# Kernel tuning notes

Hardware: AMD Instinct MI355X
Metric: run time of the kernel (lower is better)

The kernel has to match this reference:

```python
import jax, jax.numpy as jnp
import numpy as np

B, S, H, FD, FL = 2, 2048, 1024, 3072, 3072
MAX_SPAN = 30
LAM = 0.4
MAX_K = int(S * LAM)  # static upper bound on top-k spans (819)
NEG = -10000.0
LN_EPS = 1e-5


def _mlp(x, W, b, g, be):
    # FullyConnectedLayer: Linear -> GELU(erf) -> LayerNorm (dropout = eval identity)
    h = jax.nn.gelu(x @ W + b, approximate=False)
    mu = jnp.mean(h, axis=-1, keepdims=True)
    var = jnp.var(h, axis=-1, keepdims=True)
    return (h - mu) / jnp.sqrt(var + LN_EPS) * g + be


def _mask_tensor(t, m):
    # s2e mask_tensor: additive -1e4 on masked entries, then clamp
    return jnp.clip(t + (1.0 - m) * NEG, NEG, -NEG)


def setup_inputs() -> dict:
    key = jax.random.key(0)
    ks = iter(jax.random.split(key, 32))
    w = lambda shape: jax.random.normal(next(ks), shape, jnp.float32) * 0.02
    inp = {
        "input_emb": jax.random.normal(next(ks), (B, S, H), jnp.float32),
        "input_masks": jnp.ones((B, S), jnp.int32),
    }
    for p, F in [("sm", FD), ("em", FD), ("sc", FL), ("ec", FL)]:
        inp[p + "_W"] = w((H, F))
        inp[p + "_b"] = jnp.zeros((F,), jnp.float32)
        inp[p + "_g"] = jnp.ones((F,), jnp.float32)
        inp[p + "_be"] = jnp.zeros((F,), jnp.float32)
    inp["cls_s_W"] = w((FD,)); inp["cls_s_b"] = jnp.zeros((), jnp.float32)
    inp["cls_e_W"] = w((FD,)); inp["cls_e_b"] = jnp.zeros((), jnp.float32)
    inp["s2e_W"] = w((FD, FD)); inp["s2e_b"] = jnp.zeros((FD,), jnp.float32)
    for p in ["a_ss", "a_ee", "a_se", "a_es"]:
        inp[p + "_W"] = w((FL, FL))
        inp[p + "_b"] = jnp.zeros((FL,), jnp.float32)
    return inp


def reference(input_emb, input_masks,
              sm_W, sm_b, sm_g, sm_be, em_W, em_b, em_g, em_be,
              sc_W, sc_b, sc_g, sc_be, ec_W, ec_b, ec_g, ec_be,
              cls_s_W, cls_s_b, cls_e_W, cls_e_b, s2e_W, s2e_b,
              a_ss_W, a_ss_b, a_ee_W, a_ee_b, a_se_W, a_se_b, a_es_W, a_es_b):
    # start/end representations
    sm = _mlp(input_emb, sm_W, sm_b, sm_g, sm_be)  # [B,S,FD]
    em = _mlp(input_emb, em_W, em_b, em_g, em_be)  # [B,S,FD]
    sc = _mlp(input_emb, sc_W, sc_b, sc_g, sc_be)  # [B,S,FL]
    ec = _mlp(input_emb, ec_W, ec_b, ec_g, ec_be)  # [B,S,FL]

    # mention scores: joint bilinear + broadcast start/end unary scores
    s_sc = sm @ cls_s_W + cls_s_b  # [B,S]
    e_sc = em @ cls_e_W + cls_e_b  # [B,S]
    joint = jnp.einsum('bsd,btd->bst', sm @ s2e_W + s2e_b, em)  # [B,S,S]
    mention = joint + s_sc[:, :, None] + e_sc[:, None, :]

    # triu(0) & tril(max_span_len-1) band mask
    ii = jnp.arange(S)
    d = ii[None, :] - ii[:, None]  # end - start
    band = ((d >= 0) & (d < MAX_SPAN)).astype(mention.dtype)
    mention = _mask_tensor(mention, band[None])

    # top-k over flattened S*S scores, per-example k via span_mask
    k = (input_masks.sum(-1).astype(jnp.float32) * LAM).astype(jnp.int32)  # [B]
    flat = mention.reshape(B, -1)
    _, top_idx = jax.lax.top_k(flat, MAX_K)  # [B,MAX_K]
    span_mask = (jnp.arange(MAX_K)[None, :] < k[:, None]).astype(jnp.int32)
    idx = top_idx * span_mask + (1 - span_mask) * (S * S - 1)
    sidx = jnp.sort(idx, axis=-1)
    starts = sidx // S  # [B,MAX_K]
    ends = sidx % S
    tms = jnp.take_along_axis(flat, sidx, axis=-1)  # [B,MAX_K]
    pair = tms[:, :, None] + tms[:, None, :]  # [B,MAX_K,MAX_K]

    # gather coref reps at top-k span boundaries
    tks = jnp.take_along_axis(sc, starts[:, :, None], axis=1)  # [B,MAX_K,FL]
    tke = jnp.take_along_axis(ec, ends[:, :, None], axis=1)    # [B,MAX_K,FL]

    coref = (jnp.einsum('bkd,bjd->bkj', tks @ a_ss_W + a_ss_b, tks)
             + jnp.einsum('bkd,bjd->bkj', tke @ a_ee_W + a_ee_b, tke)
             + jnp.einsum('bkd,bjd->bkj', tks @ a_se_W + a_se_b, tke)
             + jnp.einsum('bkd,bjd->bkj', tke @ a_es_W + a_es_b, tks))

    final = pair + coref
    amask = jnp.tril(jnp.ones((MAX_K, MAX_K), final.dtype), -1)[None]
    amask = amask * span_mask[:, :, None].astype(final.dtype)
    final = _mask_tensor(final, amask)
    final = jnp.concatenate([final, jnp.zeros((B, MAX_K, 1), final.dtype)], axis=-1)
    return final
```

## Files before the change

### kernel.cpp

```cpp
#include <hip/hip_runtime.h>
#include <hip/hip_bf16.h>
#include <math.h>

#define S_LEN 2048
#define BATCH 2
#define HDIM 1024
#define FDIM 3072
#define MAXK 819
#define MAXSPAN 30
#define NEGV -10000.0f

typedef __attribute__((ext_vector_type(8))) short short8;
typedef __attribute__((ext_vector_type(4))) float f32x4;
typedef __hip_bfloat16 hb;

__device__ __forceinline__ float gelu_f(float x) {
  return 0.5f * x * (1.0f + erff(x * 0.70710678118654752440f));
}

__device__ __forceinline__ unsigned short bf_bits(float x) {
  hb b = __float2bfloat16(x);
  return *reinterpret_cast<unsigned short*>(&b);
}
__device__ __forceinline__ float bf_back(unsigned short u) {
  hb b = *reinterpret_cast<hb*>(&u);
  return __bfloat162float(b);
}

__device__ __forceinline__ void gload16(const void* g, void* l) {
  __builtin_amdgcn_global_load_lds(
      (const __attribute__((address_space(1))) void*)g,
      (__attribute__((address_space(3))) void*)l, 16, 0, 0);
}

__global__ __launch_bounds__(256) void gemm_fast1(
    const hb* __restrict__ A, const hb* __restrict__ B,
    const float* __restrict__ bias, const float* __restrict__ bias2,
    void* __restrict__ Cv,
    int M, int N, int K, int lda, int ldb, int ldc,
    long long sA, long long sB, long long sC,
    int act, int out_mode, int kspl)
{
  const int zb = blockIdx.z / kspl, zk = blockIdx.z - zb * kspl;
  A += (long long)zb * sA + (long long)zk * K;
  B += (long long)zb * sB + (long long)zk * K;
  const long long cbase = (long long)blockIdx.z * sC;
  const float* bp = (bias2 && zb) ? bias2 : bias;
  const int bm = blockIdx.y * 128, bn = blockIdx.x * 128;
  const int tid = threadIdx.x;
  const int lane = tid & 63;
  const int wv = tid >> 6, wr = wv >> 1, wc = wv & 1;
  const int lrow = lane & 15, lk = lane >> 4;
  __shared__ __align__(16) hb As[128 * 128];
  __shared__ __align__(16) hb Bs[128 * 128];

  const int srow = tid >> 4;
  const int sc8 = tid & 15;
  const int sslot = (sc8 - srow) & 15;

  f32x4 acc[4][4];
#pragma unroll
  for (int mi = 0; mi < 4; ++mi)
#pragma unroll
    for (int ni = 0; ni < 4; ++ni) acc[mi][ni] = (f32x4){0.f, 0.f, 0.f, 0.f};

  long long aoff[8], boff[8];
#pragma unroll
  for (int it = 0; it < 8; ++it) {
    int gm = bm + srow + it * 16; if (gm > M - 1) gm = M - 1;
    int gn = bn + srow + it * 16; if (gn > N - 1) gn = N - 1;
    aoff[it] = (long long)gm * lda + sslot * 8;
    boff[it] = (long long)gn * ldb + sslot * 8;
  }

  for (int k0 = 0; k0 < K; k0 += 128) {
#pragma unroll
    for (int it = 0; it < 8; ++it)
      gload16(A + aoff[it] + k0, &As[(tid + it * 256) * 8]);
#pragma unroll
    for (int it = 0; it < 8; ++it)
      gload16(B + boff[it] + k0, &Bs[(tid + it * 256) * 8]);
    __syncthreads();
#pragma unroll
    for (int ks = 0; ks < 4; ++ks) {
      const int sa = ((ks * 4 + lk + lrow) & 15) * 8;
      short8 a[4], b[4];
#pragma unroll
      for (int mi = 0; mi < 4; ++mi)
        a[mi] = *(const short8*)&As[(wr * 64 + mi * 16 + lrow) * 128 + sa];
#pragma unroll
      for (int ni = 0; ni < 4; ++ni)
        b[ni] = *(const short8*)&Bs[(wc * 64 + ni * 16 + lrow) * 128 + sa];
#pragma unroll
      for (int mi = 0; mi < 4; ++mi)
#pragma unroll
        for (int ni = 0; ni < 4; ++ni)
          acc[mi][ni] = __builtin_amdgcn_mfma_f32_16x16x32_bf16(
              a[mi], b[ni], acc[mi][ni], 0, 0, 0);
    }
    __syncthreads();
  }

  float* Cf = (float*)Cv;
  hb* Cb = (hb*)Cv;
#pragma unroll
  for (int mi = 0; mi < 4; ++mi) {
#pragma unroll
    for (int ni = 0; ni < 4; ++ni) {
#pragma unroll
      for (int q = 0; q < 4; ++q) {
        int gm = bm + wr * 64 + mi * 16 + lk * 4 + q;
        int gn = bn + wc * 64 + ni * 16 + lrow;
        if (gm < M && gn < N) {
          float v = acc[mi][ni][q];
          if (bp)   v += bp[gn];
          if (act)  v = gelu_f(v);
          long long off = cbase + (long long)gm * ldc + gn;
          if (out_mode == 1) Cb[off] = __float2bfloat16(v);
          else               Cf[off] = v;
        }
      }
    }
  }
}

__global__ __launch_bounds__(256) void gemm_fast3(
    const hb* __restrict__ Ah, const hb* __restrict__ Al,
    const hb* __restrict__ Bh, const hb* __restrict__ Bl,
    const float* __restrict__ bias, void* __restrict__ Cv, void* __restrict__ Cv2,
    int M, int N, int K, int lda, int ldb, int ldc, int act, int out_mode)
{
  const int bm = blockIdx.y * 128, bn = blockIdx.x * 128;
  const int tid = threadIdx.x;
  const int lane = tid & 63;
  const int wv = tid >> 6, wr = wv >> 1, wc = wv & 1;
  const int lrow = lane & 15, lk = lane >> 4;
  __shared__ __align__(16) hb AsH[128 * 64];
  __shared__ __align__(16) hb AsL[128 * 64];
  __shared__ __align__(16) hb BsH[128 * 64];
  __shared__ __align__(16) hb BsL[128 * 64];

  const int srow = tid >> 3;
  const int sc8 = tid & 7;
  const int sslot = (sc8 - srow) & 7;

  f32x4 acc[4][4];
#pragma unroll
  for (int mi = 0; mi < 4; ++mi)
#pragma unroll
    for (int ni = 0; ni < 4; ++ni) acc[mi][ni] = (f32x4){0.f, 0.f, 0.f, 0.f};

  long long aoff[4], boff[4];
#pragma unroll
  for (int it = 0; it < 4; ++it) {
    int gm = bm + srow + it * 32; if (gm > M - 1) gm = M - 1;
    int gn = bn + srow + it * 32; if (gn > N - 1) gn = N - 1;
    aoff[it] = (long long)gm * lda + sslot * 8;
    boff[it] = (long long)gn * ldb + sslot * 8;
  }

  for (int k0 = 0; k0 < K; k0 += 64) {
#pragma unroll
    for (int it = 0; it < 4; ++it) {
      gload16(Ah + aoff[it] + k0, &AsH[(tid + it * 256) * 8]);
      gload16(Al + aoff[it] + k0, &AsL[(tid + it * 256) * 8]);
      gload16(Bh + boff[it] + k0, &BsH[(tid + it * 256) * 8]);
      gload16(Bl + boff[it] + k0, &BsL[(tid + it * 256) * 8]);
    }
    __syncthreads();
#pragma unroll
    for (int ks = 0; ks < 2; ++ks) {
      const int sa = ((ks * 4 + lk + lrow) & 7) * 8;
      short8 aH[4], aL[4], bH[4], bL[4];
#pragma unroll
      for (int mi = 0; mi < 4; ++mi) {
        int r = (wr * 64 + mi * 16 + lrow) * 64 + sa;
        aH[mi] = *(const short8*)&AsH[r];
        aL[mi] = *(const short8*)&AsL[r];
      }
#pragma unroll
      for (int ni = 0; ni < 4; ++ni) {
        int r = (wc * 64 + ni * 16 + lrow) * 64 + sa;
        bH[ni] = *(const short8*)&BsH[r];
        bL[ni] = *(const short8*)&BsL[r];
      }
#pragma unroll
      for (int mi = 0; mi < 4; ++mi)
#pragma unroll
        for (int ni = 0; ni < 4; ++ni) {
          acc[mi][ni] = __builtin_amdgcn_mfma_f32_16x16x32_bf16(
              aH[mi], bH[ni], acc[mi][ni], 0, 0, 0);
          acc[mi][ni] = __builtin_amdgcn_mfma_f32_16x16x32_bf16(
              aL[mi], bH[ni], acc[mi][ni], 0, 0, 0);
          acc[mi][ni] = __builtin_amdgcn_mfma_f32_16x16x32_bf16(
              aH[mi], bL[ni], acc[mi][ni], 0, 0, 0);
        }
    }
    __syncthreads();
  }

  float* Cf = (float*)Cv;
  hb* Cb = (hb*)Cv;
  hb* Cb2 = (hb*)Cv2;
#pragma unroll
  for (int mi = 0; mi < 4; ++mi) {
#pragma unroll
    for (int ni = 0; ni < 4; ++ni) {
#pragma unroll
      for (int q = 0; q < 4; ++q) {
        int gm = bm + wr * 64 + mi * 16 + lk * 4 + q;
        int gn = bn + wc * 64 + ni * 16 + lrow;
        if (gm < M && gn < N) {
          float v = acc[mi][ni][q];
          if (bias) v += bias[gn];
          if (act)  v = gelu_f(v);
          long long off = (long long)gm * ldc + gn;
          if (out_mode == 2) {
            unsigned short h = bf_bits(v);
            unsigned short l = bf_bits(v - bf_back(h));
            Cb[off] = *reinterpret_cast<hb*>(&h);
            Cb2[off] = *reinterpret_cast<hb*>(&l);
          } else {
            Cf[off] = v;
          }
        }
      }
    }
  }
}

__global__ __launch_bounds__(256) void bandmm(
    const hb* __restrict__ Phi, const hb* __restrict__ Plo,
    const hb* __restrict__ Ehi, const hb* __restrict__ Elo,
    float* __restrict__ partial)
{
  const int s0 = blockIdx.x * 64;
  const int kq = blockIdx.y;
  const int b = blockIdx.z;
  const int tid = threadIdx.x;
  const int lane = tid & 63;
  const int wv = tid >> 6, wr = wv >> 1, wc = wv & 1;
  const int lrow = lane & 15, lk = lane >> 4;
  __shared__ __align__(16) hb As[64 * 64];
  __shared__ __align__(16) hb Bs[96 * 64];

  f32x4 acc[2][3];
#pragma unroll
  for (int mi = 0; mi < 2; ++mi)
#pragma unroll
    for (int ni = 0; ni < 3; ++ni) acc[mi][ni] = (f32x4){0.f, 0.f, 0.f, 0.f};

  const long long Pbase = (long long)(b * S_LEN) * FDIM;
  long long aoff[2], boff[3];
#pragma unroll
  for (int it = 0; it < 2; ++it) {
    int row = (tid + it * 256) >> 3;
    aoff[it] = Pbase + (long long)(s0 + row) * FDIM + (tid & 7) * 8;
  }
#pragma unroll
  for (int it = 0; it < 3; ++it) {
    int row = (tid + it * 256) >> 3;
    int t = s0 + row; if (t > S_LEN - 1) t = S_LEN - 1;
    boff[it] = Pbase + (long long)t * FDIM + (tid & 7) * 8;
  }

  const int kbeg = kq * (FDIM / 4), kend = kbeg + FDIM / 4;
  for (int t3 = 0; t3 < 3; ++t3) {
    const hb* Ap = (t3 == 1) ? Plo : Phi;
    const hb* Bp = (t3 == 2) ? Elo : Ehi;
    for (int k0 = kbeg; k0 < kend; k0 += 64) {
#pragma unroll
      for (int it = 0; it < 2; ++it)
        gload16(Ap + aoff[it] + k0, &As[(tid + it * 256) * 8]);
#pragma unroll
      for (int it = 0; it < 3; ++it)
        gload16(Bp + boff[it] + k0, &Bs[(tid + it * 256) * 8]);
      __syncthreads();
#pragma unroll
      for (int ks = 0; ks < 2; ++ks) {
        short8 a[2], bb[3];
#pragma unroll
        for (int mi = 0; mi < 2; ++mi)
          a[mi] = *(const short8*)&As[(wr * 32 + mi * 16 + lrow) * 64 + ks * 32 + lk * 8];
#pragma unroll
        for (int ni = 0; ni < 3; ++ni)
          bb[ni] = *(const short8*)&Bs[(wc * 48 + ni * 16 + lrow) * 64 + ks * 32 + lk * 8];
#pragma unroll
        for (int mi = 0; mi < 2; ++mi)
#pragma unroll
          for (int ni = 0; ni < 3; ++ni)
            acc[mi][ni] = __builtin_amdgcn_mfma_f32_16x16x32_bf16(
                a[mi], bb[ni], acc[mi][ni], 0, 0, 0);
      }
      __syncthreads();
    }
  }

#pragma unroll
  for (int mi = 0; mi < 2; ++mi) {
#pragma unroll
    for (int ni = 0; ni < 3; ++ni) {
#pragma unroll
      for (int q = 0; q < 4; ++q) {
        int i = wr * 32 + mi * 16 + lk * 4 + q;
        int n = wc * 48 + ni * 16 + lrow;
        int d = n - i;
        if (d >= 0 && d < 32) {
          long long off = (((long long)(kq * 2 + b)) * S_LEN + (s0 + i)) * 32 + d;
          partial[off] = acc[mi][ni][q];
        }
      }
    }
  }
}

__global__ __launch_bounds__(256) void band_reduce(
    const float* __restrict__ partial, const float* __restrict__ ssc,
    const float* __restrict__ esc, float* __restrict__ band)
{
  int idx = blockIdx.x * 256 + threadIdx.x;
  if (idx >= BATCH * S_LEN * 32) return;
  int d = idx & 31;
  int s = (idx >> 5) & (S_LEN - 1);
  int b = idx >> 16;
  int t = s + d;
  float v;
  if (d < MAXSPAN && t < S_LEN) {
    float sum = 0.f;
#pragma unroll
    for (int kq = 0; kq < 4; ++kq)
      sum += partial[(((long long)(kq * 2 + b)) * S_LEN + s) * 32 + d];
    sum += ssc[b * S_LEN + s] + esc[b * S_LEN + t];
    v = fminf(fmaxf(sum, NEGV), -NEGV);
  } else {
    v = -3.0e38f;
  }
  band[idx] = v;
}

__global__ __launch_bounds__(256) void prep_split(
    const float* __restrict__ emb, hb* __restrict__ hi, hb* __restrict__ lo,
    long long n4, int nb_split,
    const float* __restrict__ W, hb* __restrict__ WhiT, hb* __restrict__ WloT,
    int K, int N)
{
  if ((int)blockIdx.x < nb_split) {
    long long i = (long long)blockIdx.x * 256 + threadIdx.x;
    if (i >= n4) return;
    float4 v = ((const float4*)emb)[i];
    unsigned short h[4], l[4];
    float vv[4] = {v.x, v.y, v.z, v.w};
#pragma unroll
    for (int j = 0; j < 4; ++j) {
      h[j] = bf_bits(vv[j]);
      l[j] = bf_bits(vv[j] - bf_back(h[j]));
    }
    ((uint2*)hi)[i] = *(uint2*)h;
    ((uint2*)lo)[i] = *(uint2*)l;
    return;
  }
  __shared__ float t[32][33];
  int idx = blockIdx.x - nb_split;
  int xb = idx % (N / 32), yb = idx / (N / 32);
  int k0 = yb * 32, n0 = xb * 32;
  int tx = threadIdx.x & 31, ty = threadIdx.x >> 5;
#pragma unroll
  for (int r = 0; r < 4; ++r)
    t[ty + r * 8][tx] = W[(long long)(k0 + ty + r * 8) * N + (n0 + tx)];
  __syncthreads();
#pragma unroll
  for (int r = 0; r < 4; ++r) {
    int n = n0 + ty + r * 8;
    float v = t[tx][ty + r * 8];
    unsigned short h = bf_bits(v);
    unsigned short l = bf_bits(v - bf_back(h));
    WhiT[(long long)n * K + k0 + tx] = *reinterpret_cast<hb*>(&h);
    WloT[(long long)n * K + k0 + tx] = *reinterpret_cast<hb*>(&l);
  }
}

__global__ __launch_bounds__(256) void splitT_mat(
    const float* __restrict__ src, hb* __restrict__ hiT, hb* __restrict__ loT,
    int K, int N)
{
  __shared__ float t[32][33];
  int k0 = blockIdx.y * 32, n0 = blockIdx.x * 32;
  int tx = threadIdx.x & 31, ty = threadIdx.x >> 5;
#pragma unroll
  for (int r = 0; r < 4; ++r)
    t[ty + r * 8][tx] = src[(long long)(k0 + ty + r * 8) * N + (n0 + tx)];
  __syncthreads();
#pragma unroll
  for (int r = 0; r < 4; ++r) {
    int n = n0 + ty + r * 8;
    float v = t[tx][ty + r * 8];
    unsigned short h = bf_bits(v);
    unsigned short l = bf_bits(v - bf_back(h));
    hiT[(long long)n * K + k0 + tx] = *reinterpret_cast<hb*>(&h);
    loT[(long long)n * K + k0 + tx] = *reinterpret_cast<hb*>(&l);
  }
}

__global__ __launch_bounds__(256) void ln_split_dot(
    const float* __restrict__ src, hb* __restrict__ hi, hb* __restrict__ lo,
    const float* __restrict__ g, const float* __restrict__ be,
    const float* __restrict__ w, const float* __restrict__ wb,
    float* __restrict__ dot_out)
{
  __shared__ float row[FDIM];
  __shared__ double scr[4];
  __shared__ double sh_mu, sh_rstd;
  const long long r = blockIdx.x;
  const float* p = src + r * FDIM;
  const int tid = threadIdx.x;

  double s = 0.0;
#pragma unroll
  for (int pp = 0; pp < 3; ++pp) {
    int c4 = pp * 256 + tid;
    float4 v = *(const float4*)(p + c4 * 4);
    *(float4*)&row[c4 * 4] = v;
    s += (double)v.x + (double)v.y + (double)v.z + (double)v.w;
  }
#pragma unroll
  for (int off = 32; off; off >>= 1) s += __shfl_down(s, off, 64);
  if ((tid & 63) == 0) scr[tid >> 6] = s;
  __syncthreads();
  if (tid == 0) sh_mu = (scr[0] + scr[1] + scr[2] + scr[3]) / FDIM;
  __syncthreads();
  double mu = sh_mu;
  double vs = 0.0;
#pragma unroll
  for (int pp = 0; pp < 12; ++pp) {
    double d = (double)row[pp * 256 + tid] - mu;
    vs += d * d;
  }
#pragma unroll
  for (int off = 32; off; off >>= 1) vs += __shfl_down(vs, off, 64);
  __syncthreads();
  if ((tid & 63) == 0) scr[tid >> 6] = vs;
  __syncthreads();
  if (tid == 0)
    sh_rstd = 1.0 / sqrt((scr[0] + scr[1] + scr[2] + scr[3]) / FDIM + 1e-5);
  __syncthreads();
  double rstd = sh_rstd;

  double dot = 0.0;
#pragma unroll
  for (int pp = 0; pp < 3; ++pp) {
    int c4 = pp * 256 + tid;
    float4 gv = *(const float4*)(g + c4 * 4);
    float4 bv = *(const float4*)(be + c4 * 4);
    float4 wv = *(const float4*)(w + c4 * 4);
    float xv[4];
    *(float4*)xv = *(const float4*)&row[c4 * 4];
    unsigned short hh[4], ll[4];
    float gg[4] = {gv.x, gv.y, gv.z, gv.w};
    float bb[4] = {bv.x, bv.y, bv.z, bv.w};
    float ww[4] = {wv.x, wv.y, wv.z, wv.w};
#pragma unroll
    for (int j = 0; j < 4; ++j) {
      float val = (float)(((double)xv[j] - mu) * rstd * (double)gg[j] + (double)bb[j]);
      dot += (double)val * (double)ww[j];
      hh[j] = bf_bits(val);
      ll[j] = bf_bits(val - bf_back(hh[j]));
    }
    *(uint2*)(hi + r * FDIM + c4 * 4) = *(uint2*)hh;
    *(uint2*)(lo + r * FDIM + c4 * 4) = *(uint2*)ll;
  }
#pragma unroll
  for (int off = 32; off; off >>= 1) dot += __shfl_down(dot, off, 64);
  __syncthreads();
  if ((tid & 63) == 0) scr[tid >> 6] = dot;
  __syncthreads();
  if (tid == 0)
    dot_out[r] = (float)(scr[0] + scr[1] + scr[2] + scr[3] + (double)wb[0]);
}

__global__ __launch_bounds__(256) void ln_rows_bf2(
    const float* __restrict__ src0, const float* __restrict__ src1,
    hb* __restrict__ dst0, hb* __restrict__ dst1,
    const float* __restrict__ g0, const float* __restrict__ g1,
    const float* __restrict__ be0, const float* __restrict__ be1,
    int n, long long lds_, long long ldd)
{
  const int sel = blockIdx.y;
  long long r = blockIdx.x;
  const float* p = (sel ? src1 : src0) + r * lds_;
  hb* d = (sel ? dst1 : dst0) + r * ldd;
  const float* g = sel ? g1 : g0;
  const float* be = sel ? be1 : be0;
  __shared__ double scratch[4];
  __shared__ double sh_mu, sh_rstd;
  double s = 0.0;
  for (int c = threadIdx.x; c < n; c += 256) s += (double)p[c];
#pragma unroll
  for (int off = 32; off; off >>= 1) s += __shfl_down(s, off, 64);
  if ((threadIdx.x & 63) == 0) scratch[threadIdx.x >> 6] = s;
  __syncthreads();
  if (threadIdx.x == 0) sh_mu = (scratch[0] + scratch[1] + scratch[2] + scratch[3]) / n;
  __syncthreads();
  double mu = sh_mu;
  double vs = 0.0;
  for (int c = threadIdx.x; c < n; c += 256) { double dd = (double)p[c] - mu; vs += dd * dd; }
#pragma unroll
  for (int off = 32; off; off >>= 1) vs += __shfl_down(vs, off, 64);
  __syncthreads();
  if ((threadIdx.x & 63) == 0) scratch[threadIdx.x >> 6] = vs;
  __syncthreads();
  if (threadIdx.x == 0)
    sh_rstd = 1.0 / sqrt((scratch[0] + scratch[1] + scratch[2] + scratch[3]) / n + 1e-5);
  __syncthreads();
  double rstd = sh_rstd;
  for (int c = threadIdx.x; c < n; c += 256)
    d[c] = __float2bfloat16(
        (float)(((double)p[c] - mu) * rstd * (double)g[c] + (double)be[c]));
}

__device__ __forceinline__ unsigned f2k(float f) {
  unsigned u = __float_as_uint(f);
  return (u & 0x80000000u) ? ~u : (u | 0x80000000u);
}

__device__ void bitonic1024(int* a) {
  const int tid = threadIdx.x;
  for (int sz = 2; sz <= 1024; sz <<= 1) {
    for (int st = sz >> 1; st > 0; st >>= 1) {
      __syncthreads();
      int j = tid ^ st;
      if (j > tid) {
        int x = a[tid], y = a[j];
        bool asc = (tid & sz) == 0;
        if ((x > y) == asc) { a[tid] = y; a[j] = x; }
      }
    }
  }
  __syncthreads();
}

__global__ __launch_bounds__(1024) void select_sort(
    const float* __restrict__ band, const int* __restrict__ masks,
    int* __restrict__ sidx, int* __restrict__ starts, int* __restrict__ ends,
    float* __restrict__ tms, int* __restrict__ kvals)
{
  const int b = blockIdx.x;
  const int tid = threadIdx.x;
  __shared__ int hist[256];
  __shared__ int sel[1024];
  __shared__ int eq[1024];
  __shared__ int sred[16];
  __shared__ int cvar[4];
  __shared__ int cnt_gt, cnt_eq;

  int msum = 0;
  for (int i = tid; i < S_LEN; i += 1024) msum += masks[b * S_LEN + i];
#pragma unroll
  for (int off = 32; off; off >>= 1) msum += __shfl_down(msum, off, 64);
  if ((tid & 63) == 0) sred[tid >> 6] = msum;
  __syncthreads();
  if (tid == 0) {
    int t = 0;
    for (int w = 0; w < 16; ++w) t += sred[w];
    cvar[2] = t;
  }
  __syncthreads();
  int kv = (int)((float)cvar[2] * 0.4f);
  if (kv > MAXK) kv = MAXK;
  if (kv < 0) kv = 0;

  const float* bb = band + (long long)b * (S_LEN * 32);
  const float4* b4 = (const float4*)bb;
  const int N4 = S_LEN * 8;
  unsigned prefix = 0u;
  int remaining = kv;

  if (kv > 0) {
    for (int byte = 3; byte >= 0; --byte) {
      if (tid < 256) hist[tid] = 0;
      __syncthreads();
      for (int i = tid; i < N4; i += 1024) {
        float4 v = b4[i];
        float vv[4] = {v.x, v.y, v.z, v.w};
#pragma unroll
        for (int j = 0; j < 4; ++j) {
          unsigned key = f2k(vv[j]);
          bool match = (byte == 3) ||
              ((key >> ((byte + 1) * 8)) == (prefix >> ((byte + 1) * 8)));
          if (match) atomicAdd(&hist[(key >> (byte * 8)) & 255], 1);
        }
      }
      __syncthreads();
      if (tid == 0) {
        int cum = 0, chosen = 255;
        for (int v = 255; v >= 0; --v) {
          int h = hist[v];
          if (cum + h >= remaining) { chosen = v; cvar[0] = remaining - cum; break; }
          cum += h;
        }
        cvar[1] = chosen;
      }
      __syncthreads();
      remaining = cvar[0];
      prefix |= ((unsigned)cvar[1]) << (byte * 8);
      __syncthreads();
    }
    if (tid == 0) { cnt_gt = 0; cnt_eq = 0; }
    __syncthreads();
    for (int i = tid; i < N4; i += 1024) {
      float4 v = b4[i];
      float vv[4] = {v.x, v.y, v.z, v.w};
#pragma unroll
      for (int j = 0; j < 4; ++j) {
        unsigned key = f2k(vv[j]);
        if (key < prefix) continue;
        int e = i * 4 + j;
        int s = e >> 5, d = e & 31;
        int flat = s * S_LEN + s + d;
        if (key > prefix) {
          int p = atomicAdd(&cnt_gt, 1);
          if (p < MAXK) sel[p] = flat;
        } else {
          int p = atomicAdd(&cnt_eq, 1);
          if (p < 1024) eq[p] = flat;
        }
      }
    }
    __syncthreads();
    int ngt = cnt_gt;
    int neq = cnt_eq; if (neq > 1024) neq = 1024;
    if (tid >= neq) eq[tid] = 0x7FFFFFFF;
    __syncthreads();
    bitonic1024(eq);
    int need = kv - ngt;
    if (tid < need) sel[ngt + tid] = eq[tid];
    __syncthreads();
  }
  if (tid >= kv && tid < MAXK) sel[tid] = S_LEN * S_LEN - 1;
  if (tid >= MAXK) sel[tid] = 0x7FFFFFFF;
  __syncthreads();
  bitonic1024(sel);
  if (tid < MAXK) {
    int idx = sel[tid];
    int s = idx >> 11;
    int t = idx & (S_LEN - 1);
    sidx[b * MAXK + tid] = idx;
    starts[b * MAXK + tid] = s;
    ends[b * MAXK + tid] = t;
    tms[b * MAXK + tid] = band[((long long)(b * S_LEN + s)) * 32 + (t - s)];
  }
  if (tid == 0) kvals[b] = kv;
}

__global__ __launch_bounds__(256) void gather_bf2(
    const float* __restrict__ src,
    const int* __restrict__ rows0, const int* __restrict__ rows1,
    hb* __restrict__ dst0, hb* __restrict__ dst1)
{
  int g = blockIdx.x;
  int b = g / MAXK;
  const int* rows = blockIdx.y ? rows1 : rows0;
  hb* dst = blockIdx.y ? dst1 : dst0;
  int r = rows[g];
  const float4* s4 = (const float4*)(src + ((long long)(b * S_LEN + r)) * HDIM);
  hb* d = dst + (long long)g * HDIM;
  float4 v = s4[threadIdx.x];
  d[threadIdx.x * 4 + 0] = __float2bfloat16(v.x);
  d[threadIdx.x * 4 + 1] = __float2bfloat16(v.y);
  d[threadIdx.x * 4 + 2] = __float2bfloat16(v.z);
  d[threadIdx.x * 4 + 3] = __float2bfloat16(v.w);
}

__global__ __launch_bounds__(256) void wprep(
    const float* __restrict__ a0W, const float* __restrict__ a1W,
    const float* __restrict__ a2W, const float* __restrict__ a3W,
    hb* __restrict__ Wq1t, hb* __restrict__ Wq2t,
    const float* __restrict__ scW, const float* __restrict__ ecW,
    hb* __restrict__ scWt, hb* __restrict__ ecWt,
    const float* __restrict__ b0, const float* __restrict__ b1,
    const float* __restrict__ b2, const float* __restrict__ b3,
    float* __restrict__ biasq)
{
  const int z = blockIdx.z;
  int tx = threadIdx.x & 31, ty = threadIdx.x >> 5;
  if (z < 4) {
    if ((int)blockIdx.y >= FDIM / 32) return;
    __shared__ float t[32][33];
    const float* src = (z == 0) ? a0W : (z == 1) ? a1W : (z == 2) ? a2W : a3W;
    hb* dst = (z < 2) ? Wq1t : Wq2t;
    const int koff = (z & 1) * FDIM;
    int k0 = blockIdx.y * 32, n0 = blockIdx.x * 32;
#pragma unroll
    for (int r = 0; r < 4; ++r)
      t[ty + r * 8][tx] = src[(long long)(k0 + ty + r * 8) * FDIM + (n0 + tx)];
    __syncthreads();
#pragma unroll
    for (int r = 0; r < 4; ++r) {
      int n = n0 + ty + r * 8;
      dst[(long long)n * (2 * FDIM) + koff + k0 + tx] =
          __float2bfloat16(t[tx][ty + r * 8]);
    }
  } else {
    int yy = blockIdx.y;
    if (yy < 64) {
      __shared__ float t[32][33];
      const float* src = (yy < 32) ? scW : ecW;
      hb* dst = (yy < 32) ? scWt : ecWt;
      int k0 = (yy & 31) * 32, n0 = blockIdx.x * 32;
#pragma unroll
      for (int r = 0; r < 4; ++r)
        t[ty + r * 8][tx] = src[(long long)(k0 + ty + r * 8) * FDIM + (n0 + tx)];
      __syncthreads();
#pragma unroll
      for (int r = 0; r < 4; ++r) {
        int n = n0 + ty + r * 8;
        dst[(long long)n * HDIM + k0 + tx] = __float2bfloat16(t[tx][ty + r * 8]);
      }
    } else if (yy == 64 && blockIdx.x < 24) {
      int i = blockIdx.x * 256 + threadIdx.x;
      if (i < FDIM) biasq[i] = b0[i] + b1[i];
      else          biasq[i] = b2[i - FDIM] + b3[i - FDIM];
    }
  }
}

__global__ __launch_bounds__(256) void final_assemble(
    const float* __restrict__ coref4, const float* __restrict__ tms,
    const int* __restrict__ kvals, float* __restrict__ out)
{
  const long long SL = (long long)MAXK * MAXK;
  int g = blockIdx.x;
  int b = g / MAXK;
  int i = g - b * MAXK;
  int kv = kvals[b];
  float ti = tms[g];
  const float* crow = coref4 + (long long)(b * 4) * SL + (long long)i * MAXK;
  float* orow = out + (long long)b * MAXK * (MAXK + 1) + (long long)i * (MAXK + 1);
  for (int j = threadIdx.x; j < MAXK + 1; j += 256) {
    float v;
    if (j == MAXK) v = 0.f;
    else {
      float c = ((crow[j] + crow[j + SL]) + (crow[j + 2 * SL] + crow[j + 3 * SL]));
      v = ti + tms[b * MAXK + j] + c;
      if (!((j < i) && (i < kv))) v += NEGV;
      v = fminf(fmaxf(v, NEGV), -NEGV);
    }
    orow[j] = v;
  }
}

static inline void launch1(const hb* A, const hb* B,
    const float* bias, const float* bias2, void* C,
    int M, int N, int K, int lda, int ldb, int ldc,
    long long sA, long long sB, long long sC,
    int act, int out_mode, int zcount, int kspl, hipStream_t stream)
{
  dim3 grid((N + 127) / 128, (M + 127) / 128, zcount);
  gemm_fast1<<<grid, 256, 0, stream>>>(A, B, bias, bias2, C, M, N, K,
                                       lda, ldb, ldc, sA, sB, sC,
                                       act, out_mode, kspl);
}

static inline void launch3(const hb* Ah, const hb* Al, const hb* Bh, const hb* Bl,
    const float* bias, void* C, void* C2, int M, int N, int K,
    int lda, int ldb, int ldc, int act, int out_mode, hipStream_t stream)
{
  dim3 grid((N + 127) / 128, (M + 127) / 128, 1);
  gemm_fast3<<<grid, 256, 0, stream>>>(Ah, Al, Bh, Bl, bias, C, C2,
                                       M, N, K, lda, ldb, ldc, act, out_mode);
}

extern "C" void kernel_launch(void* const* d_in, const int* in_sizes, int n_in,
                              void* d_out, int out_size, void* d_ws, size_t ws_size,
                              hipStream_t stream) {
  const float* input_emb = (const float*)d_in[0];
  const int*   input_masks = (const int*)d_in[1];
  const float* sm_W = (const float*)d_in[2];
  const float* sm_b = (const float*)d_in[3];
  const float* sm_g = (const float*)d_in[4];
  const float* sm_be = (const float*)d_in[5];
  const float* em_W = (const float*)d_in[6];
  const float* em_b = (const float*)d_in[7];
  const float* em_g = (const float*)d_in[8];
  const float* em_be = (const float*)d_in[9];
  const float* sc_W = (const float*)d_in[10];
  const float* sc_b = (const float*)d_in[11];
  const float* sc_g = (const float*)d_in[12];
  const float* sc_be = (const float*)d_in[13];
  const float* ec_W = (const float*)d_in[14];
  const float* ec_b = (const float*)d_in[15];
  const float* ec_g = (const float*)d_in[16];
  const float* ec_be = (const float*)d_in[17];
  const float* cls_s_W = (const float*)d_in[18];
  const float* cls_s_b = (const float*)d_in[19];
  const float* cls_e_W = (const float*)d_in[20];
  const float* cls_e_b = (const float*)d_in[21];
  const float* s2e_W = (const float*)d_in[22];
  const float* s2e_b = (const float*)d_in[23];
  const float* a_ss_W = (const float*)d_in[24];
  const float* a_ss_b = (const float*)d_in[25];
  const float* a_ee_W = (const float*)d_in[26];
  const float* a_ee_b = (const float*)d_in[27];
  const float* a_se_W = (const float*)d_in[28];
  const float* a_se_b = (const float*)d_in[29];
  const float* a_es_W = (const float*)d_in[30];
  const float* a_es_b = (const float*)d_in[31];
  float* out = (float*)d_out;

  const int NROW = BATCH * S_LEN;
  const int MROW = BATCH * MAXK;
  const long long SZ_BIG = (long long)NROW * FDIM * 4;

  char* ws = (char*)d_ws;
  float* smF    = (float*)(ws);
  hb* sm_hi     = (hb*)(ws + 50331648LL);
  hb* sm_lo     = (hb*)(ws + 75497472LL);
  hb* emb_hi    = (hb*)(ws + 100663296LL);
  hb* emb_lo    = (hb*)(ws + 109051904LL);
  hb* w1_hiT    = (hb*)(ws + 117440512LL);
  hb* w1_loT    = (hb*)(ws + 123731968LL);
  hb* s2e_hiT   = (hb*)(ws);
  hb* s2e_loT   = (hb*)(ws + 18874368LL);
  hb* proj_hi   = (hb*)(ws + 100663296LL);
  hb* proj_lo   = (hb*)(ws + 125829120LL);
  hb* emb2_hi   = (hb*)(ws);
  hb* emb2_lo   = (hb*)(ws + 8388608LL);
  hb* w2_hiT    = (hb*)(ws + 16777216LL);
  hb* w2_loT    = (hb*)(ws + 23068672LL);
  float* emF    = (float*)(ws + 50331648LL);
  hb* em_hi     = (hb*)(ws);
  hb* em_lo     = (hb*)(ws + 25165824LL);
  float* partial = (float*)(ws + 50331648LL);
  hb* Wq1t  = (hb*)(ws);
  hb* Wq2t  = (hb*)(ws + 37748736LL);
  hb* tkcat = (hb*)(ws + 75497472LL);
  hb* qcat  = (hb*)(ws + 95625216LL);
  float* coref4 = (float*)(ws + 115752960LL);
  float* mlp_s = (float*)(ws + 95625216LL);
  float* mlp_e = (float*)(ws + 115752960LL);
  hb* Xs_bf = (hb*)(ws + 75497472LL);
  hb* Xe_bf = (hb*)(ws + 78852096LL);
  hb* scWt  = (hb*)(ws + 82206720LL);
  hb* ecWt  = (hb*)(ws + 88498176LL);
  const long long P = 3 * SZ_BIG;
  float* band = (float*)(ws + P);
  float* ssc  = (float*)(ws + P + 524288);
  float* esc  = (float*)(ws + P + 540672);
  int* sidx   = (int*)(ws + P + 557056);
  int* starts = (int*)(ws + P + 565248);
  int* ends   = (int*)(ws + P + 573440);
  float* tms  = (float*)(ws + P + 581632);
  int* kvals  = (int*)(ws + P + 589824);
  float* biasq1 = (float*)(ws + P + 590080);
  float* biasq2 = (float*)(ws + P + 602368);
  (void)biasq2;
  if (ws_size < (size_t)(P + 614656)) return;

  const long long n4_emb = (long long)NROW * HDIM / 4;
  const int nb_split = (int)((n4_emb + 255) / 256);
  const int nb_T = (FDIM / 32) * (HDIM / 32);

  prep_split<<<nb_split + nb_T, 256, 0, stream>>>(
      input_emb, emb_hi, emb_lo, n4_emb, nb_split, sm_W, w1_hiT, w1_loT, HDIM, FDIM);
  launch3(emb_hi, emb_lo, w1_hiT, w1_loT, sm_b, smF, nullptr,
          NROW, FDIM, HDIM, HDIM, HDIM, FDIM, 1, 0, stream);
  ln_split_dot<<<NROW, 256, 0, stream>>>(smF, sm_hi, sm_lo, sm_g, sm_be,
                                         cls_s_W, cls_s_b, ssc);
  splitT_mat<<<dim3(FDIM / 32, FDIM / 32), 256, 0, stream>>>(s2e_W, s2e_hiT, s2e_loT, FDIM, FDIM);
  launch3(sm_hi, sm_lo, s2e_hiT, s2e_loT, s2e_b, proj_hi, proj_lo,
          NROW, FDIM, FDIM, FDIM, FDIM, FDIM, 0, 2, stream);
  prep_split<<<nb_split + nb_T, 256, 0, stream>>>(
      input_emb, emb2_hi, emb2_lo, n4_emb, nb_split, em_W, w2_hiT, w2_loT, HDIM, FDIM);
  launch3(emb2_hi, emb2_lo, w2_hiT, w2_loT, em_b, emF, nullptr,
          NROW, FDIM, HDIM, HDIM, HDIM, FDIM, 1, 0, stream);
  ln_split_dot<<<NROW, 256, 0, stream>>>(emF, em_hi, em_lo, em_g, em_be,
                                         cls_e_W, cls_e_b, esc);
  bandmm<<<dim3(S_LEN / 64, 4, BATCH), 256, 0, stream>>>(proj_hi, proj_lo, em_hi, em_lo, partial);
  band_reduce<<<(BATCH * S_LEN * 32) / 256, 256, 0, stream>>>(partial, ssc, esc, band);
  select_sort<<<BATCH, 1024, 0, stream>>>(band, input_masks, sidx, starts, ends, tms, kvals);

  gather_bf2<<<dim3(MROW, 2), 256, 0, stream>>>(input_emb, starts, ends, Xs_bf, Xe_bf);

  wprep<<<dim3(FDIM / 32, FDIM / 32 + 1, 5), 256, 0, stream>>>(
      a_ss_W, a_es_W, a_se_W, a_ee_W, Wq1t, Wq2t,
      sc_W, ec_W, scWt, ecWt,
      a_ss_b, a_es_b, a_se_b, a_ee_b, biasq1);

  launch1(Xs_bf, scWt, sc_b, ec_b, mlp_s, MROW, FDIM, HDIM, HDIM, HDIM, FDIM,
          (long long)MROW * HDIM, (long long)FDIM * HDIM, (long long)MROW * FDIM,
          1, 0, 2, 1, stream);

  ln_rows_bf2<<<dim3(MROW, 2), 256, 0, stream>>>(
      mlp_s, mlp_e, tkcat, tkcat + FDIM, sc_g, ec_g, sc_be, ec_be,
      FDIM, FDIM, 2 * FDIM);

  launch1(tkcat, Wq1t, biasq1, nullptr, qcat, MROW, 2 * FDIM, 2 * FDIM,
          2 * FDIM, 2 * FDIM, 2 * FDIM, 0, 0, 0, 0, 1, 1, 1, stream);

  launch1(qcat, tkcat, nullptr, nullptr, coref4, MAXK, MAXK, 1536,
          2 * FDIM, 2 * FDIM, MAXK,
          (long long)MAXK * 2 * FDIM, (long long)MAXK * 2 * FDIM,
          (long long)MAXK * MAXK, 0, 0, BATCH * 4, 4, stream);

  final_assemble<<<MROW, 256, 0, stream>>>(coref4, tms, kvals, out);
}
```

Before: 1.207 ms.

## Fuse band reduce into select_sort, gather into wprep, widen transpose tiles

Folds the band_reduce kernel into the start of select_sort and the top-k row gather into an extra z-slice of wprep, which removes two kernel launches. The weight transpose and split kernels now use 64x32 tiles and write packed pairs of bf16 values as 32-bit stores in place of single 16-bit stores. The cost is that the band reduction now runs in only two blocks (one per batch) where it used to span many blocks, which could serialise that work.

```diff
diff --git a/kernel.cpp b/kernel.cpp
--- a/kernel.cpp
+++ b/kernel.cpp
@@ -314,30 +314,6 @@
   }
 }
 
-__global__ __launch_bounds__(256) void band_reduce(
-    const float* __restrict__ partial, const float* __restrict__ ssc,
-    const float* __restrict__ esc, float* __restrict__ band)
-{
-  int idx = blockIdx.x * 256 + threadIdx.x;
-  if (idx >= BATCH * S_LEN * 32) return;
-  int d = idx & 31;
-  int s = (idx >> 5) & (S_LEN - 1);
-  int b = idx >> 16;
-  int t = s + d;
-  float v;
-  if (d < MAXSPAN && t < S_LEN) {
-    float sum = 0.f;
-#pragma unroll
-    for (int kq = 0; kq < 4; ++kq)
-      sum += partial[(((long long)(kq * 2 + b)) * S_LEN + s) * 32 + d];
-    sum += ssc[b * S_LEN + s] + esc[b * S_LEN + t];
-    v = fminf(fmaxf(sum, NEGV), -NEGV);
-  } else {
-    v = -3.0e38f;
-  }
-  band[idx] = v;
-}
-
 __global__ __launch_bounds__(256) void prep_split(
     const float* __restrict__ emb, hb* __restrict__ hi, hb* __restrict__ lo,
     long long n4, int nb_split,
@@ -359,23 +335,29 @@
     ((uint2*)lo)[i] = *(uint2*)l;
     return;
   }
-  __shared__ float t[32][33];
+  __shared__ float t[64][33];
   int idx = blockIdx.x - nb_split;
-  int xb = idx % (N / 32), yb = idx / (N / 32);
-  int k0 = yb * 32, n0 = xb * 32;
+  int nbx = N / 32;
+  int xb = idx % nbx, yb = idx / nbx;
+  int k0 = yb * 64, n0 = xb * 32;
+  if (k0 >= K) return;
   int tx = threadIdx.x & 31, ty = threadIdx.x >> 5;
 #pragma unroll
-  for (int r = 0; r < 4; ++r)
+  for (int r = 0; r < 8; ++r)
     t[ty + r * 8][tx] = W[(long long)(k0 + ty + r * 8) * N + (n0 + tx)];
   __syncthreads();
 #pragma unroll
   for (int r = 0; r < 4; ++r) {
     int n = n0 + ty + r * 8;
-    float v = t[tx][ty + r * 8];
-    unsigned short h = bf_bits(v);
-    unsigned short l = bf_bits(v - bf_back(h));
-    WhiT[(long long)n * K + k0 + tx] = *reinterpret_cast<hb*>(&h);
-    WloT[(long long)n * K + k0 + tx] = *reinterpret_cast<hb*>(&l);
+    float v0 = t[tx * 2][ty + r * 8];
+    float v1 = t[tx * 2 + 1][ty + r * 8];
+    unsigned short h0 = bf_bits(v0), h1 = bf_bits(v1);
+    unsigned short l0 = bf_bits(v0 - bf_back(h0));
+    unsigned short l1 = bf_bits(v1 - bf_back(h1));
+    ((unsigned*)(WhiT + (long long)n * K + k0))[tx] =
+        (unsigned)h0 | ((unsigned)h1 << 16);
+    ((unsigned*)(WloT + (long long)n * K + k0))[tx] =
+        (unsigned)l0 | ((unsigned)l1 << 16);
   }
 }
 
@@ -383,21 +365,25 @@
     const float* __restrict__ src, hb* __restrict__ hiT, hb* __restrict__ loT,
     int K, int N)
 {
-  __shared__ float t[32][33];
-  int k0 = blockIdx.y * 32, n0 = blockIdx.x * 32;
+  __shared__ float t[64][33];
+  int k0 = blockIdx.y * 64, n0 = blockIdx.x * 32;
   int tx = threadIdx.x & 31, ty = threadIdx.x >> 5;
 #pragma unroll
-  for (int r = 0; r < 4; ++r)
+  for (int r = 0; r < 8; ++r)
     t[ty + r * 8][tx] = src[(long long)(k0 + ty + r * 8) * N + (n0 + tx)];
   __syncthreads();
 #pragma unroll
   for (int r = 0; r < 4; ++r) {
     int n = n0 + ty + r * 8;
-    float v = t[tx][ty + r * 8];
-    unsigned short h = bf_bits(v);
-    unsigned short l = bf_bits(v - bf_back(h));
-    hiT[(long long)n * K + k0 + tx] = *reinterpret_cast<hb*>(&h);
-    loT[(long long)n * K + k0 + tx] = *reinterpret_cast<hb*>(&l);
+    float v0 = t[tx * 2][ty + r * 8];
+    float v1 = t[tx * 2 + 1][ty + r * 8];
+    unsigned short h0 = bf_bits(v0), h1 = bf_bits(v1);
+    unsigned short l0 = bf_bits(v0 - bf_back(h0));
+    unsigned short l1 = bf_bits(v1 - bf_back(h1));
+    ((unsigned*)(hiT + (long long)n * K + k0))[tx] =
+        (unsigned)h0 | ((unsigned)h1 << 16);
+    ((unsigned*)(loT + (long long)n * K + k0))[tx] =
+        (unsigned)l0 | ((unsigned)l1 << 16);
   }
 }
 
@@ -539,7 +525,9 @@
 }
 
 __global__ __launch_bounds__(1024) void select_sort(
-    const float* __restrict__ band, const int* __restrict__ masks,
+    const float* __restrict__ partial, const float* __restrict__ ssc,
+    const float* __restrict__ esc, float* __restrict__ band,
+    const int* __restrict__ masks,
     int* __restrict__ sidx, int* __restrict__ starts, int* __restrict__ ends,
     float* __restrict__ tms, int* __restrict__ kvals)
 {
@@ -552,6 +540,26 @@
   __shared__ int cvar[4];
   __shared__ int cnt_gt, cnt_eq;
 
+  float* bw = band + (long long)b * (S_LEN * 32);
+  for (int idx = tid; idx < S_LEN * 32; idx += 1024) {
+    int d = idx & 31;
+    int s = idx >> 5;
+    int tt = s + d;
+    float v;
+    if (d < MAXSPAN && tt < S_LEN) {
+      float sum = 0.f;
+#pragma unroll
+      for (int kq = 0; kq < 4; ++kq)
+        sum += partial[(((long long)(kq * 2 + b)) * S_LEN + s) * 32 + d];
+      sum += ssc[b * S_LEN + s] + esc[b * S_LEN + tt];
+      v = fminf(fmaxf(sum, NEGV), -NEGV);
+    } else {
+      v = -3.0e38f;
+    }
+    bw[idx] = v;
+  }
+  __syncthreads();
+
   int msum = 0;
   for (int i = tid; i < S_LEN; i += 1024) msum += masks[b * S_LEN + i];
 #pragma unroll
@@ -568,8 +576,7 @@
   if (kv > MAXK) kv = MAXK;
   if (kv < 0) kv = 0;
 
-  const float* bb = band + (long long)b * (S_LEN * 32);
-  const float4* b4 = (const float4*)bb;
+  const float4* b4 = (const float4*)bw;
   const int N4 = S_LEN * 8;
   unsigned prefix = 0u;
   int remaining = kv;
@@ -651,25 +658,6 @@
   if (tid == 0) kvals[b] = kv;
 }
 
-__global__ __launch_bounds__(256) void gather_bf2(
-    const float* __restrict__ src,
-    const int* __restrict__ rows0, const int* __restrict__ rows1,
-    hb* __restrict__ dst0, hb* __restrict__ dst1)
-{
-  int g = blockIdx.x;
-  int b = g / MAXK;
-  const int* rows = blockIdx.y ? rows1 : rows0;
-  hb* dst = blockIdx.y ? dst1 : dst0;
-  int r = rows[g];
-  const float4* s4 = (const float4*)(src + ((long long)(b * S_LEN + r)) * HDIM);
-  hb* d = dst + (long long)g * HDIM;
-  float4 v = s4[threadIdx.x];
-  d[threadIdx.x * 4 + 0] = __float2bfloat16(v.x);
-  d[threadIdx.x * 4 + 1] = __float2bfloat16(v.y);
-  d[threadIdx.x * 4 + 2] = __float2bfloat16(v.z);
-  d[threadIdx.x * 4 + 3] = __float2bfloat16(v.w);
-}
-
 __global__ __launch_bounds__(256) void wprep(
     const float* __restrict__ a0W, const float* __restrict__ a1W,
     const float* __restrict__ a2W, const float* __restrict__ a3W,
@@ -678,48 +666,70 @@
     hb* __restrict__ scWt, hb* __restrict__ ecWt,
     const float* __restrict__ b0, const float* __restrict__ b1,
     const float* __restrict__ b2, const float* __restrict__ b3,
-    float* __restrict__ biasq)
-{
+    float* __restrict__ biasq,
+    const float* __restrict__ emb,
+    const int* __restrict__ starts, const int* __restrict__ ends,
+    hb* __restrict__ Xs, hb* __restrict__ Xe)
+{
+  __shared__ float t[64][33];
   const int z = blockIdx.z;
   int tx = threadIdx.x & 31, ty = threadIdx.x >> 5;
   if (z < 4) {
-    if ((int)blockIdx.y >= FDIM / 32) return;
-    __shared__ float t[32][33];
+    if ((int)blockIdx.y >= FDIM / 64) return;
     const float* src = (z == 0) ? a0W : (z == 1) ? a1W : (z == 2) ? a2W : a3W;
     hb* dst = (z < 2) ? Wq1t : Wq2t;
     const int koff = (z & 1) * FDIM;
-    int k0 = blockIdx.y * 32, n0 = blockIdx.x * 32;
-#pragma unroll
-    for (int r = 0; r < 4; ++r)
+    int k0 = blockIdx.y * 64, n0 = blockIdx.x * 32;
+#pragma unroll
+    for (int r = 0; r < 8; ++r)
       t[ty + r * 8][tx] = src[(long long)(k0 + ty + r * 8) * FDIM + (n0 + tx)];
     __syncthreads();
 #pragma unroll
     for (int r = 0; r < 4; ++r) {
       int n = n0 + ty + r * 8;
-      dst[(long long)n * (2 * FDIM) + koff + k0 + tx] =
-          __float2bfloat16(t[tx][ty + r * 8]);
-    }
-  } else {
+      float v0 = t[tx * 2][ty + r * 8];
+      float v1 = t[tx * 2 + 1][ty + r * 8];
+      ((unsigned*)(dst + (long long)n * (2 * FDIM) + koff + k0))[tx] =
+          (unsigned)bf_bits(v0) | ((unsigned)bf_bits(v1) << 16);
+    }
+  } else if (z == 4) {
     int yy = blockIdx.y;
-    if (yy < 64) {
-      __shared__ float t[32][33];
-      const float* src = (yy < 32) ? scW : ecW;
-      hb* dst = (yy < 32) ? scWt : ecWt;
-      int k0 = (yy & 31) * 32, n0 = blockIdx.x * 32;
-#pragma unroll
-      for (int r = 0; r < 4; ++r)
+    if (yy < 32) {
+      const float* src = (yy < 16) ? scW : ecW;
+      hb* dst = (yy < 16) ? scWt : ecWt;
+      int k0 = (yy & 15) * 64, n0 = blockIdx.x * 32;
+#pragma unroll
+      for (int r = 0; r < 8; ++r)
         t[ty + r * 8][tx] = src[(long long)(k0 + ty + r * 8) * FDIM + (n0 + tx)];
       __syncthreads();
 #pragma unroll
       for (int r = 0; r < 4; ++r) {
         int n = n0 + ty + r * 8;
-        dst[(long long)n * HDIM + k0 + tx] = __float2bfloat16(t[tx][ty + r * 8]);
-      }
-    } else if (yy == 64 && blockIdx.x < 24) {
+        float v0 = t[tx * 2][ty + r * 8];
+        float v1 = t[tx * 2 + 1][ty + r * 8];
+        ((unsigned*)(dst + (long long)n * HDIM + k0))[tx] =
+            (unsigned)bf_bits(v0) | ((unsigned)bf_bits(v1) << 16);
+      }
+    } else if (yy == 32 && blockIdx.x < 24) {
       int i = blockIdx.x * 256 + threadIdx.x;
       if (i < FDIM) biasq[i] = b0[i] + b1[i];
       else          biasq[i] = b2[i - FDIM] + b3[i - FDIM];
     }
+  } else {
+    const int MR = BATCH * MAXK;
+    int u = blockIdx.y * (FDIM / 32) + blockIdx.x;
+    if (u >= 2 * MR) return;
+    int which = u >= MR;
+    int g = u - which * MR;
+    int b = g / MAXK;
+    const int* rows = which ? ends : starts;
+    hb* dst = which ? Xe : Xs;
+    int r = rows[g];
+    float4 v = ((const float4*)(emb + ((long long)(b * S_LEN + r)) * HDIM))[threadIdx.x];
+    unsigned plo = (unsigned)bf_bits(v.x) | ((unsigned)bf_bits(v.y) << 16);
+    unsigned phi = (unsigned)bf_bits(v.z) | ((unsigned)bf_bits(v.w) << 16);
+    uint2 pk; pk.x = plo; pk.y = phi;
+    ((uint2*)(dst + (long long)g * HDIM))[threadIdx.x] = pk;
   }
 }
 
@@ -857,7 +867,7 @@
 
   const long long n4_emb = (long long)NROW * HDIM / 4;
   const int nb_split = (int)((n4_emb + 255) / 256);
-  const int nb_T = (FDIM / 32) * (HDIM / 32);
+  const int nb_T = (FDIM / 32) * (HDIM / 64);
 
   prep_split<<<nb_split + nb_T, 256, 0, stream>>>(
       input_emb, emb_hi, emb_lo, n4_emb, nb_split, sm_W, w1_hiT, w1_loT, HDIM, FDIM);
@@ -865,7 +875,7 @@
           NROW, FDIM, HDIM, HDIM, HDIM, FDIM, 1, 0, stream);
   ln_split_dot<<<NROW, 256, 0, stream>>>(smF, sm_hi, sm_lo, sm_g, sm_be,
                                          cls_s_W, cls_s_b, ssc);
-  splitT_mat<<<dim3(FDIM / 32, FDIM / 32), 256, 0, stream>>>(s2e_W, s2e_hiT, s2e_loT, FDIM, FDIM);
+  splitT_mat<<<dim3(FDIM / 32, FDIM / 64), 256, 0, stream>>>(s2e_W, s2e_hiT, s2e_loT, FDIM, FDIM);
   launch3(sm_hi, sm_lo, s2e_hiT, s2e_loT, s2e_b, proj_hi, proj_lo,
           NROW, FDIM, FDIM, FDIM, FDIM, FDIM, 0, 2, stream);
   prep_split<<<nb_split + nb_T, 256, 0, stream>>>(
@@ -875,15 +885,14 @@
   ln_split_dot<<<NROW, 256, 0, stream>>>(emF, em_hi, em_lo, em_g, em_be,
                                          cls_e_W, cls_e_b, esc);
   bandmm<<<dim3(S_LEN / 64, 4, BATCH), 256, 0, stream>>>(proj_hi, proj_lo, em_hi, em_lo, partial);
-  band_reduce<<<(BATCH * S_LEN * 32) / 256, 256, 0, stream>>>(partial, ssc, esc, band);
-  select_sort<<<BATCH, 1024, 0, stream>>>(band, input_masks, sidx, starts, ends, tms, kvals);
-
-  gather_bf2<<<dim3(MROW, 2), 256, 0, stream>>>(input_emb, starts, ends, Xs_bf, Xe_bf);
-
-  wprep<<<dim3(FDIM / 32, FDIM / 32 + 1, 5), 256, 0, stream>>>(
+  select_sort<<<BATCH, 1024, 0, stream>>>(partial, ssc, esc, band, input_masks,
+                                          sidx, starts, ends, tms, kvals);
+
+  wprep<<<dim3(FDIM / 32, FDIM / 64, 6), 256, 0, stream>>>(
       a_ss_W, a_es_W, a_se_W, a_ee_W, Wq1t, Wq2t,
       sc_W, ec_W, scWt, ecWt,
-      a_ss_b, a_es_b, a_se_b, a_ee_b, biasq1);
+      a_ss_b, a_es_b, a_se_b, a_ee_b, biasq1,
+      input_emb, starts, ends, Xs_bf, Xe_bf);
 
   launch1(Xs_bf, scWt, sc_b, ec_b, mlp_s, MROW, FDIM, HDIM, HDIM, HDIM, FDIM,
           (long long)MROW * HDIM, (long long)FDIM * HDIM, (long long)MROW * FDIM,
```

Result: slower. 1.233 ms (+2.2%).
